# Performance work log

Measured on AMD Instinct MI355X. Metric: run time of the kernel, lower is better.

Reference implementation:

```python
import jax, jax.numpy as jnp
import numpy as np

EPS = 1e-5

def knn_gather(x, k):
    # x: [B,N,C] -> neighbors [B,N,k,C] (k nearest incl. self, DGCNN style)
    sq = jnp.sum(x * x, axis=-1)                                   # [B,N]
    dist = sq[:, :, None] + sq[:, None, :] - 2.0 * jnp.einsum('bnc,bmc->bnm', x, x)
    _, idx = jax.lax.top_k(-dist, k)                               # [B,N,k]
    neigh = jax.vmap(lambda xb, ib: xb[ib])(x, idx)                # [B,N,k,C]
    return neigh

def local_cov(neigh):
    # neigh: [B,N,k,C] -> flattened per-point covariance [B,N,C*C]
    k = neigh.shape[2]
    c = neigh - jnp.mean(neigh, axis=2, keepdims=True)
    cov = jnp.einsum('bnkc,bnkd->bncd', c, c) / k
    return cov.reshape(cov.shape[0], cov.shape[1], -1)

def bn(x, g, b):
    # BatchNorm1d training-mode forward on [B,N,C]: stats over (B,N), biased var
    m = jnp.mean(x, axis=(0, 1))
    v = jnp.var(x, axis=(0, 1))
    return (x - m) * jax.lax.rsqrt(v + EPS) * g + b

def setup_inputs() -> dict:
    key = jax.random.key(0)
    ks = jax.random.split(key, 8)
    B, N = 2, 8192
    d = {}
    d['x'] = jax.random.normal(ks[0], (B, N, 3), dtype=jnp.float32)
    # conv weights stored as [in, out] (1x1 Conv1d == per-point matmul)
    def w(k_, i, o):
        return jax.random.normal(k_, (i, o), dtype=jnp.float32) * (1.0 / np.sqrt(i))
    d['W1'] = w(ks[1], 12, 64);   d['g1'] = jnp.ones(64);   d['b1'] = jnp.zeros(64)
    d['W2'] = w(ks[2], 64, 64);   d['g2'] = jnp.ones(64);   d['b2'] = jnp.zeros(64)
    d['W3'] = w(ks[3], 64, 64);   d['g3'] = jnp.ones(64);   d['b3'] = jnp.zeros(64)
    d['gW1'] = w(ks[4], 64, 128);  d['gg1'] = jnp.ones(128);  d['gb1'] = jnp.zeros(128)
    d['gW2'] = w(ks[5], 128, 1024); d['gg2'] = jnp.ones(1024); d['gb2'] = jnp.zeros(1024)
    d['W4'] = w(ks[6], 1024, 512); d['g4'] = jnp.ones(512);  d['b4'] = jnp.zeros(512)
    return d

def reference(x, W1, g1, b1, W2, g2, b2, W3, g3, b3,
              gW1, gg1, gb1, gW2, gg2, gb2, W4, g4, b4):
    # GBEncoder forward
    neigh = knn_gather(x, 32)                                   # [B,N,32,3]
    h = jnp.concatenate([x, local_cov(neigh)], axis=-1)         # [B,N,12]
    h = jax.nn.relu(bn(h @ W1, g1, b1))                         # [B,N,64]
    h = jax.nn.relu(bn(h @ W2, g2, b2))
    h = jax.nn.relu(bn(h @ W3, g3, b3))
    # GraphLayer 1: knn(k=8) gather -> max over neighbors -> 1x1 conv + BN + LeakyReLU
    n = jnp.max(knn_gather(h, 8), axis=2)                       # [B,N,64]
    h = jax.nn.leaky_relu(bn(n @ gW1, gg1, gb1), 0.01)          # [B,N,128]
    # GraphLayer 2
    n = jnp.max(knn_gather(h, 8), axis=2)                       # [B,N,128]
    h = jax.nn.leaky_relu(bn(n @ gW2, gg2, gb2), 0.01)          # [B,N,1024]
    # global max-pool over points, keepdim -> [B,1,1024]
    h = jnp.max(h, axis=1, keepdims=True)
    return jax.nn.relu(bn(h @ W4, g4, b4))                      # [B,1,512]
```

## Files before the change

### kernel.cpp

```cpp
#include <hip/hip_runtime.h>
#include <cfloat>
#include <cstdint>

#define NPTS 8192
#define NBROWS 16384

typedef unsigned long long u64;

__device__ __forceinline__ unsigned fkey(float f) {
  unsigned u = __float_as_uint(f);
  return (u & 0x80000000u) ? ~u : (u | 0x80000000u);
}
__device__ __forceinline__ float fdecode(unsigned k) {
  unsigned u = (k & 0x80000000u) ? (k ^ 0x80000000u) : ~k;
  return __uint_as_float(u);
}

template <int K>
__device__ __forceinline__ void chain_insert(u64 (&kk)[K], u64 key) {
  #pragma unroll
  for (int q = K - 1; q >= 1; --q) {
    bool cm1 = key < kk[q - 1];
    bool cq  = key < kk[q];
    kk[q] = cm1 ? kk[q - 1] : (cq ? key : kk[q]);
  }
  kk[0] = (key < kk[0]) ? key : kk[0];
}

__global__ __launch_bounds__(256) void sqx_kernel(const float* __restrict__ x,
                                                  float* __restrict__ sq) {
  int r = blockIdx.x * 256 + threadIdx.x;
  const float* xp = x + (size_t)r * 3;
  sq[r] = fmaf(xp[2], xp[2], fmaf(xp[1], xp[1], xp[0] * xp[0]));
}

__global__ __launch_bounds__(512, 4) void knn32_cov_kernel(const float* __restrict__ x,
                                                           const float* __restrict__ sqx,
                                                           float* __restrict__ feat) {
  __shared__ __align__(16) unsigned char smem[78080];
  float4* stage4 = (float4*)smem;
  unsigned* keyArea = (unsigned*)smem;
  unsigned* Trow = (unsigned*)(smem + 67584);
  unsigned* cnt  = (unsigned*)(smem + 67712);
  u64* apb = (u64*)(smem + 67840);

  const int t = threadIdx.x;
  const int r = t & 31, sub = t >> 5;
  const int rowBase = blockIdx.x * 32;
  const int batchBase = rowBase & ~(NPTS - 1);
  const int gRow = rowBase + r;

  const float xi0 = x[(size_t)gRow * 3 + 0];
  const float xi1 = x[(size_t)gRow * 3 + 1];
  const float xi2 = x[(size_t)gRow * 3 + 2];
  const float sqi = sqx[gRow];

  unsigned K[32];
  #pragma unroll
  for (int q = 0; q < 32; ++q) K[q] = 0xFFFFFFFFu;

  for (int round = 0; round < 4; ++round) {
    __syncthreads();
    #pragma unroll
    for (int u = 0; u < 4; ++u) {
      int pp = t + 512 * u;
      int s = pp >> 7, jj = pp & 127;
      int j = s * 512 + round * 128 + jj;
      const float* xp = x + (size_t)(batchBase + j) * 3;
      float4 w;
      w.x = xp[0]; w.y = xp[1]; w.z = xp[2];
      w.w = sqx[batchBase + j];
      stage4[pp] = w;
    }
    __syncthreads();
    const float4* st = stage4 + sub * 128;
    for (int jj = 0; jj < 128; ++jj) {
      float4 w = st[jj];
      float dot = fmaf(xi2, w.z, fmaf(xi1, w.y, xi0 * w.x));
      float d = sqi + w.w - 2.0f * dot;
      unsigned key = fkey(d);
      #pragma unroll
      for (int q = 31; q >= 1; --q) K[q] = max(K[q - 1], min(key, K[q]));
      K[0] = min(key, K[0]);
    }
  }
  __syncthreads();
  {
    const int base = (sub * 32 + r) * 33;
    #pragma unroll
    for (int z = 0; z < 32; ++z) keyArea[base + z] = K[z];
  }
  __syncthreads();
  if (t < 32) {
    cnt[t] = 0u;
    unsigned P[16];
    #pragma unroll
    for (int s = 0; s < 16; ++s) P[s] = 0u;
    unsigned T = 0u;
    for (int step = 0; step < 32; ++step) {
      unsigned best = 0xFFFFFFFFu; int bs = 0;
      #pragma unroll
      for (int s = 0; s < 16; ++s) {
        unsigned v = keyArea[(s * 32 + t) * 33 + P[s]];
        if (v < best) { best = v; bs = s; }
      }
      T = best;
      #pragma unroll
      for (int s = 0; s < 16; ++s) P[s] += (s == bs);
    }
    Trow[t] = T;
  }
  __syncthreads();
  for (int round = 0; round < 4; ++round) {
    __syncthreads();
    #pragma unroll
    for (int u = 0; u < 4; ++u) {
      int pp = t + 512 * u;
      int s = pp >> 7, jj = pp & 127;
      int j = s * 512 + round * 128 + jj;
      const float* xp = x + (size_t)(batchBase + j) * 3;
      float4 w;
      w.x = xp[0]; w.y = xp[1]; w.z = xp[2];
      w.w = sqx[batchBase + j];
      stage4[pp] = w;
    }
    __syncthreads();
    const float4* st = stage4 + sub * 128;
    const unsigned T = Trow[r];
    for (int jj = 0; jj < 128; ++jj) {
      float4 w = st[jj];
      float dot = fmaf(xi2, w.z, fmaf(xi1, w.y, xi0 * w.x));
      float d = sqi + w.w - 2.0f * dot;
      unsigned key = fkey(d);
      if (key <= T) {
        int j = sub * 512 + round * 128 + jj;
        unsigned slot = atomicAdd(&cnt[r], 1u);
        if (slot < 40u) apb[r * 40 + slot] = ((u64)key << 16) | (unsigned)j;
      }
    }
  }
  __syncthreads();
  if (t < 32) {
    int n = (int)cnt[t]; if (n > 40) n = 40;
    u64 kk[32];
    #pragma unroll
    for (int q = 0; q < 32; ++q) kk[q] = ~0ULL;
    for (int i = 0; i < n; ++i) chain_insert<32>(kk, apb[t * 40 + i]);
    float sx = 0.f, sy = 0.f, sz = 0.f;
    #pragma unroll 4
    for (int z = 0; z < 32; ++z) {
      const float* xp = x + (size_t)(batchBase + (int)(kk[z] & 0xFFFFULL)) * 3;
      sx += xp[0]; sy += xp[1]; sz += xp[2];
    }
    const float m0 = sx * (1.f / 32.f), m1 = sy * (1.f / 32.f), m2 = sz * (1.f / 32.f);
    float c00 = 0, c01 = 0, c02 = 0, c11 = 0, c12 = 0, c22 = 0;
    #pragma unroll 4
    for (int z = 0; z < 32; ++z) {
      const float* xp = x + (size_t)(batchBase + (int)(kk[z] & 0xFFFFULL)) * 3;
      float a0 = xp[0] - m0, a1 = xp[1] - m1, a2 = xp[2] - m2;
      c00 = fmaf(a0, a0, c00); c01 = fmaf(a0, a1, c01); c02 = fmaf(a0, a2, c02);
      c11 = fmaf(a1, a1, c11); c12 = fmaf(a1, a2, c12); c22 = fmaf(a2, a2, c22);
    }
    const float inv = 1.f / 32.f;
    float* fp = feat + (size_t)(rowBase + t) * 12;
    fp[0] = xi0; fp[1] = xi1; fp[2] = xi2;
    fp[3] = c00 * inv; fp[4] = c01 * inv; fp[5] = c02 * inv;
    fp[6] = c01 * inv; fp[7] = c11 * inv; fp[8] = c12 * inv;
    fp[9] = c02 * inv; fp[10] = c12 * inv; fp[11] = c22 * inv;
  }
}

__global__ __launch_bounds__(64) void mm12_64_kernel(const float* __restrict__ feat,
                                                     const float* __restrict__ W,
                                                     float* __restrict__ y,
                                                     float* __restrict__ psum,
                                                     float* __restrict__ psq) {
  __shared__ __align__(16) float Ws[12 * 64];
  const int t = threadIdx.x;
  for (int u = t; u < 192; u += 64) ((float4*)Ws)[u] = ((const float4*)W)[u];
  __syncthreads();
  const int row = blockIdx.x * 64 + t;
  float in[12];
  {
    const float4* fp = (const float4*)(feat + (size_t)row * 12);
    float4 a = fp[0], b = fp[1], c = fp[2];
    in[0] = a.x; in[1] = a.y; in[2] = a.z; in[3] = a.w;
    in[4] = b.x; in[5] = b.y; in[6] = b.z; in[7] = b.w;
    in[8] = c.x; in[9] = c.y; in[10] = c.z; in[11] = c.w;
  }
  float acc[64];
  #pragma unroll
  for (int o = 0; o < 64; ++o) acc[o] = 0.f;
  #pragma unroll
  for (int i = 0; i < 12; ++i) {
    const float xi = in[i];
    #pragma unroll
    for (int og = 0; og < 16; ++og) {
      float4 w4 = *(const float4*)(Ws + i * 64 + og * 4);
      acc[og * 4 + 0] = fmaf(xi, w4.x, acc[og * 4 + 0]);
      acc[og * 4 + 1] = fmaf(xi, w4.y, acc[og * 4 + 1]);
      acc[og * 4 + 2] = fmaf(xi, w4.z, acc[og * 4 + 2]);
      acc[og * 4 + 3] = fmaf(xi, w4.w, acc[og * 4 + 3]);
    }
  }
  float4* yp = (float4*)(y + (size_t)row * 64);
  #pragma unroll
  for (int og = 0; og < 16; ++og)
    yp[og] = make_float4(acc[og * 4 + 0], acc[og * 4 + 1], acc[og * 4 + 2], acc[og * 4 + 3]);
  #pragma unroll 1
  for (int o = 0; o < 64; ++o) {
    float s = acc[o], q = acc[o] * acc[o];
    #pragma unroll
    for (int m = 1; m < 64; m <<= 1) { s += __shfl_xor(s, m); q += __shfl_xor(q, m); }
    if (t == 0) { psum[blockIdx.x * 64 + o] = s; psq[blockIdx.x * 64 + o] = q; }
  }
}

template <int OUT, bool BNRELU>
__global__ __launch_bounds__(64) void mm64_kernel(const float* __restrict__ src,
                                                  const float* __restrict__ W,
                                                  const float* __restrict__ scale,
                                                  const float* __restrict__ shift,
                                                  float* __restrict__ y,
                                                  float* __restrict__ psum,
                                                  float* __restrict__ psq) {
  __shared__ __align__(16) float Ws[64 * OUT];
  const int t = threadIdx.x;
  for (int u = t; u < 16 * OUT; u += 64) ((float4*)Ws)[u] = ((const float4*)W)[u];
  __syncthreads();
  const int row = blockIdx.x * 64 + t;
  float in[64];
  {
    const float4* sp = (const float4*)(src + (size_t)row * 64);
    #pragma unroll
    for (int u = 0; u < 16; ++u) {
      float4 v = sp[u];
      if (BNRELU) {
        v.x = fmaxf(fmaf(v.x, scale[u * 4 + 0], shift[u * 4 + 0]), 0.f);
        v.y = fmaxf(fmaf(v.y, scale[u * 4 + 1], shift[u * 4 + 1]), 0.f);
        v.z = fmaxf(fmaf(v.z, scale[u * 4 + 2], shift[u * 4 + 2]), 0.f);
        v.w = fmaxf(fmaf(v.w, scale[u * 4 + 3], shift[u * 4 + 3]), 0.f);
      }
      in[u * 4 + 0] = v.x; in[u * 4 + 1] = v.y; in[u * 4 + 2] = v.z; in[u * 4 + 3] = v.w;
    }
  }
  for (int half = 0; half < OUT / 64; ++half) {
    float acc[64];
    #pragma unroll
    for (int o = 0; o < 64; ++o) acc[o] = 0.f;
    #pragma unroll 4
    for (int i = 0; i < 64; ++i) {
      const float xi = in[i];
      #pragma unroll
      for (int og = 0; og < 16; ++og) {
        float4 w4 = *(const float4*)(Ws + i * OUT + half * 64 + og * 4);
        acc[og * 4 + 0] = fmaf(xi, w4.x, acc[og * 4 + 0]);
        acc[og * 4 + 1] = fmaf(xi, w4.y, acc[og * 4 + 1]);
        acc[og * 4 + 2] = fmaf(xi, w4.z, acc[og * 4 + 2]);
        acc[og * 4 + 3] = fmaf(xi, w4.w, acc[og * 4 + 3]);
      }
    }
    float4* yp = (float4*)(y + (size_t)row * OUT + half * 64);
    #pragma unroll
    for (int og = 0; og < 16; ++og)
      yp[og] = make_float4(acc[og * 4 + 0], acc[og * 4 + 1], acc[og * 4 + 2], acc[og * 4 + 3]);
    #pragma unroll 1
    for (int o = 0; o < 64; ++o) {
      float s = acc[o], q = acc[o] * acc[o];
      #pragma unroll
      for (int m = 1; m < 64; m <<= 1) { s += __shfl_xor(s, m); q += __shfl_xor(q, m); }
      if (t == 0) {
        psum[blockIdx.x * OUT + half * 64 + o] = s;
        psq[blockIdx.x * OUT + half * 64 + o] = q;
      }
    }
  }
}

template <int C>
__global__ void finP_kernel(const float* __restrict__ psum, const float* __restrict__ psq,
                            const float* __restrict__ g, const float* __restrict__ b,
                            float* __restrict__ scale, float* __restrict__ shift) {
  int c = threadIdx.x;
  float s = 0.f, q = 0.f;
  for (int bb = 0; bb < 256; ++bb) { s += psum[bb * C + c]; q += psq[bb * C + c]; }
  float m = s * (1.f / 16384.f);
  float v = q * (1.f / 16384.f) - m * m;
  float sc = g[c] * rsqrtf(v + 1e-5f);
  scale[c] = sc;
  shift[c] = b[c] - m * sc;
}

template <int C, bool LEAKY>
__global__ __launch_bounds__(256) void apply_kernel(const float* __restrict__ yraw,
                                                    const float* __restrict__ scale,
                                                    const float* __restrict__ shift,
                                                    float* __restrict__ hout,
                                                    float* __restrict__ sqout) {
  const int row = blockIdx.x * 256 + threadIdx.x;
  const float4* sp = (const float4*)(yraw + (size_t)row * C);
  float4* dp = (float4*)(hout + (size_t)row * C);
  float sq = 0.f;
  #pragma unroll
  for (int u = 0; u < C / 4; ++u) {
    float4 v = sp[u];
    float4 o;
    o.x = fmaf(v.x, scale[u * 4 + 0], shift[u * 4 + 0]);
    o.y = fmaf(v.y, scale[u * 4 + 1], shift[u * 4 + 1]);
    o.z = fmaf(v.z, scale[u * 4 + 2], shift[u * 4 + 2]);
    o.w = fmaf(v.w, scale[u * 4 + 3], shift[u * 4 + 3]);
    if (LEAKY) {
      o.x = o.x > 0.f ? o.x : 0.01f * o.x;
      o.y = o.y > 0.f ? o.y : 0.01f * o.y;
      o.z = o.z > 0.f ? o.z : 0.01f * o.z;
      o.w = o.w > 0.f ? o.w : 0.01f * o.w;
    } else {
      o.x = fmaxf(o.x, 0.f); o.y = fmaxf(o.y, 0.f);
      o.z = fmaxf(o.z, 0.f); o.w = fmaxf(o.w, 0.f);
    }
    sq = fmaf(o.x, o.x, sq); sq = fmaf(o.y, o.y, sq);
    sq = fmaf(o.z, o.z, sq); sq = fmaf(o.w, o.w, sq);
    dp[u] = o;
  }
  sqout[row] = sq;
}

template <int C>
__global__ __launch_bounds__(256, 4) void knn8_kernel(const float* __restrict__ h,
                                                      const float* __restrict__ sqh,
                                                      u64* __restrict__ plist) {
  static_assert(C == 64 || C == 128, "C");
  constexpr int SMEMB = (C * 64 * 4 + 64 * 64 * 4) > 32768 ? (C * 64 * 4 + 64 * 64 * 4) : 32768;
  __shared__ __align__(16) unsigned char smem[SMEMB];
  float* As = (float*)smem;
  float* Bs = (float*)(smem + C * 64 * 4);
  __shared__ float sqAs[64];
  __shared__ float sqBs[64];
  u64* mb = (u64*)smem;

  const int t = threadIdx.x;
  const int rg = blockIdx.x >> 2, quarter = blockIdx.x & 3;
  const int rowBase = rg * 64;
  const int batchBase = rowBase & ~(NPTS - 1);
  const int tx = t & 15, ty = t >> 4;

  {
    const int ar = t & 63;
    const int k0 = (t >> 6) * (C / 4);
    const float* src = h + (size_t)(rowBase + ar) * C + k0;
    #pragma unroll
    for (int kk = 0; kk < C / 4; kk += 4) {
      float4 v = *(const float4*)(src + kk);
      As[(k0 + kk + 0) * 64 + ar] = v.x;
      As[(k0 + kk + 1) * 64 + ar] = v.y;
      As[(k0 + kk + 2) * 64 + ar] = v.z;
      As[(k0 + kk + 3) * 64 + ar] = v.w;
    }
    if (t < 64) sqAs[t] = sqh[rowBase + t];
  }

  u64 L[4][8];
  #pragma unroll
  for (int q = 0; q < 4; ++q)
    #pragma unroll
    for (int z = 0; z < 8; ++z) L[q][z] = ~0ULL;

  for (int tile = 0; tile < 32; ++tile) {
    const int colBase = quarter * 2048 + tile * 64;
    float acc[16];
    #pragma unroll
    for (int q = 0; q < 16; ++q) acc[q] = 0.f;
    for (int ch = 0; ch < C / 64; ++ch) {
      __syncthreads();
      {
        const int bc = t & 63;
        const int k0 = (t >> 6) * 16;
        const float* src = h + (size_t)(batchBase + colBase + bc) * C + ch * 64 + k0;
        #pragma unroll
        for (int kk = 0; kk < 16; kk += 4) {
          float4 v = *(const float4*)(src + kk);
          Bs[(k0 + kk + 0) * 64 + bc] = v.x;
          Bs[(k0 + kk + 1) * 64 + bc] = v.y;
          Bs[(k0 + kk + 2) * 64 + bc] = v.z;
          Bs[(k0 + kk + 3) * 64 + bc] = v.w;
        }
        if (ch == 0 && t < 64) sqBs[t] = sqh[batchBase + colBase + t];
      }
      __syncthreads();
      const float* Ab = As + ch * 64 * 64;
      #pragma unroll 4
      for (int k = 0; k < 64; ++k) {
        float4 a4 = *(const float4*)(Ab + k * 64 + ty * 4);
        float4 b4 = *(const float4*)(Bs + k * 64 + tx * 4);
        acc[0] = fmaf(a4.x, b4.x, acc[0]);   acc[1] = fmaf(a4.x, b4.y, acc[1]);
        acc[2] = fmaf(a4.x, b4.z, acc[2]);   acc[3] = fmaf(a4.x, b4.w, acc[3]);
        acc[4] = fmaf(a4.y, b4.x, acc[4]);   acc[5] = fmaf(a4.y, b4.y, acc[5]);
        acc[6] = fmaf(a4.y, b4.z, acc[6]);   acc[7] = fmaf(a4.y, b4.w, acc[7]);
        acc[8] = fmaf(a4.z, b4.x, acc[8]);   acc[9] = fmaf(a4.z, b4.y, acc[9]);
        acc[10] = fmaf(a4.z, b4.z, acc[10]); acc[11] = fmaf(a4.z, b4.w, acc[11]);
        acc[12] = fmaf(a4.w, b4.x, acc[12]); acc[13] = fmaf(a4.w, b4.y, acc[13]);
        acc[14] = fmaf(a4.w, b4.z, acc[14]); acc[15] = fmaf(a4.w, b4.w, acc[15]);
      }
    }
    #pragma unroll
    for (int q = 0; q < 4; ++q) {
      const float sa = sqAs[ty * 4 + q];
      #pragma unroll
      for (int p = 0; p < 4; ++p) {
        float d = sa + sqBs[tx * 4 + p] - 2.0f * acc[q * 4 + p];
        int j = colBase + tx * 4 + p;
        u64 key = ((u64)fkey(d) << 16) | (unsigned)j;
        chain_insert<8>(L[q], key);
      }
    }
  }
  for (int rh = 0; rh < 2; ++rh) {
    __syncthreads();
    if (ty >= rh * 8 && ty < rh * 8 + 8) {
      #pragma unroll
      for (int q = 0; q < 4; ++q) {
        int lr = (ty - rh * 8) * 4 + q;
        #pragma unroll
        for (int z = 0; z < 8; ++z) mb[(lr * 16 + tx) * 8 + z] = L[q][z];
      }
    }
    __syncthreads();
    if (t < 32) {
      int ps[16];
      #pragma unroll
      for (int s = 0; s < 16; ++s) ps[s] = 0;
      u64 outk[8];
      for (int z = 0; z < 8; ++z) {
        u64 best = ~0ULL; int bs = 0;
        #pragma unroll
        for (int s = 0; s < 16; ++s) {
          u64 v = mb[(t * 16 + s) * 8 + ps[s]];
          if (v < best) { best = v; bs = s; }
        }
        outk[z] = best;
        #pragma unroll
        for (int s = 0; s < 16; ++s) ps[s] += (s == bs);
      }
      u64* dst = plist + ((size_t)(rowBase + rh * 32 + t) * 4 + quarter) * 8;
      #pragma unroll
      for (int z = 0; z < 8; ++z) dst[z] = outk[z];
    }
  }
}

template <int C>
__global__ __launch_bounds__(256) void knn8mg_kernel(const u64* __restrict__ plist,
                                                     const float* __restrict__ h,
                                                     float* __restrict__ nout) {
  const int row = blockIdx.x * 4 + (threadIdx.x >> 6);
  const int lane = threadIdx.x & 63;
  const int batchBase = row & ~(NPTS - 1);
  const u64* A = plist + (size_t)row * 32;
  u64 kk[8];
  #pragma unroll
  for (int z = 0; z < 8; ++z) kk[z] = A[z];
  #pragma unroll
  for (int z = 8; z < 32; ++z) chain_insert<8>(kk, A[z]);
  constexpr int PER = C / 64;
  float mx[PER];
  #pragma unroll
  for (int u = 0; u < PER; ++u) mx[u] = -FLT_MAX;
  #pragma unroll
  for (int z = 0; z < 8; ++z) {
    int idx = (int)(kk[z] & 0xFFFFULL);
    const float* src = h + (size_t)(batchBase + idx) * C;
    #pragma unroll
    for (int u = 0; u < PER; ++u)
      mx[u] = fmaxf(mx[u], src[lane + u * 64]);
  }
  float* dst = nout + (size_t)row * C;
  #pragma unroll
  for (int u = 0; u < PER; ++u) dst[lane + u * 64] = mx[u];
}

__global__ __launch_bounds__(256) void mmE_kernel(const float* __restrict__ n2,
                                                  const float* __restrict__ W,
                                                  float* __restrict__ psum,
                                                  float* __restrict__ psq,
                                                  unsigned* __restrict__ gmax) {
  __shared__ __align__(16) float As[64 * 64];
  __shared__ __align__(16) float Bs[64 * 64];
  __shared__ float sP[16 * 64];
  __shared__ float qP[16 * 64];
  __shared__ float mP[16 * 64];
  const int t = threadIdx.x;
  const int rowStripe = blockIdx.x >> 4;
  const int colStripe = blockIdx.x & 15;
  const int rowBase = rowStripe * 64;
  const int colBase = colStripe * 64;
  const int batch = rowBase >> 13;
  const int tx = t & 15, ty = t >> 4;

  float acc[16];
  #pragma unroll
  for (int q = 0; q < 16; ++q) acc[q] = 0.f;

  for (int kh = 0; kh < 2; ++kh) {
    __syncthreads();
    {
      const int ar = t & 63;
      const int k0 = (t >> 6) * 16;
      const float* src = n2 + (size_t)(rowBase + ar) * 128 + kh * 64 + k0;
      #pragma unroll
      for (int kk = 0; kk < 16; kk += 4) {
        float4 v = *(const float4*)(src + kk);
        As[(k0 + kk + 0) * 64 + ar] = v.x;
        As[(k0 + kk + 1) * 64 + ar] = v.y;
        As[(k0 + kk + 2) * 64 + ar] = v.z;
        As[(k0 + kk + 3) * 64 + ar] = v.w;
      }
    }
    {
      #pragma unroll
      for (int z = 0; z < 4; ++z) {
        int u = t + 256 * z;
        int k = u >> 4, c4 = u & 15;
        float4 v = *(const float4*)(W + (size_t)(kh * 64 + k) * 1024 + colBase + c4 * 4);
        *(float4*)(Bs + k * 64 + c4 * 4) = v;
      }
    }
    __syncthreads();
    #pragma unroll 4
    for (int k = 0; k < 64; ++k) {
      float4 a4 = *(const float4*)(As + k * 64 + ty * 4);
      float4 b4 = *(const float4*)(Bs + k * 64 + tx * 4);
      acc[0] = fmaf(a4.x, b4.x, acc[0]);   acc[1] = fmaf(a4.x, b4.y, acc[1]);
      acc[2] = fmaf(a4.x, b4.z, acc[2]);   acc[3] = fmaf(a4.x, b4.w, acc[3]);
      acc[4] = fmaf(a4.y, b4.x, acc[4]);   acc[5] = fmaf(a4.y, b4.y, acc[5]);
      acc[6] = fmaf(a4.y, b4.z, acc[6]);   acc[7] = fmaf(a4.y, b4.w, acc[7]);
      acc[8] = fmaf(a4.z, b4.x, acc[8]);   acc[9] = fmaf(a4.z, b4.y, acc[9]);
      acc[10] = fmaf(a4.z, b4.z, acc[10]); acc[11] = fmaf(a4.z, b4.w, acc[11]);
      acc[12] = fmaf(a4.w, b4.x, acc[12]); acc[13] = fmaf(a4.w, b4.y, acc[13]);
      acc[14] = fmaf(a4.w, b4.z, acc[14]); acc[15] = fmaf(a4.w, b4.w, acc[15]);
    }
  }
  #pragma unroll
  for (int p = 0; p < 4; ++p) {
    float s = 0.f, q = 0.f, m = -FLT_MAX;
    #pragma unroll
    for (int qq = 0; qq < 4; ++qq) {
      float v = acc[qq * 4 + p];
      s += v; q = fmaf(v, v, q); m = fmaxf(m, v);
    }
    sP[ty * 64 + tx * 4 + p] = s;
    qP[ty * 64 + tx * 4 + p] = q;
    mP[ty * 64 + tx * 4 + p] = m;
  }
  __syncthreads();
  if (t < 64) {
    float s = 0.f, q = 0.f, m = -FLT_MAX;
    #pragma unroll
    for (int u = 0; u < 16; ++u) {
      s += sP[u * 64 + t];
      q += qP[u * 64 + t];
      m = fmaxf(m, mP[u * 64 + t]);
    }
    psum[rowStripe * 1024 + colBase + t] = s;
    psq [rowStripe * 1024 + colBase + t] = q;
    atomicMax(&gmax[batch * 1024 + colBase + t], fkey(m));
  }
}

__global__ void poolbn_kernel(const float* __restrict__ psumE, const float* __restrict__ psqE,
                              const unsigned* __restrict__ gmax,
                              const float* __restrict__ gg2, const float* __restrict__ gb2,
                              float* __restrict__ fpool) {
  int c = threadIdx.x;
  float s = 0.f, q = 0.f;
  for (int bb = 0; bb < 256; ++bb) { s += psumE[bb * 1024 + c]; q += psqE[bb * 1024 + c]; }
  float m = s * (1.f / 16384.f);
  float v = q * (1.f / 16384.f) - m * m;
  float sc = gg2[c] * rsqrtf(v + 1e-5f);
  float sh = gb2[c] - m * sc;
  #pragma unroll
  for (int b = 0; b < 2; ++b) {
    float raw = fdecode(gmax[b * 1024 + c]);
    float t = fmaf(raw, sc, sh);
    fpool[b * 1024 + c] = t > 0.f ? t : 0.01f * t;
  }
}

__global__ __launch_bounds__(64) void final_kernel(const float* __restrict__ fpool,
                                                   const float* __restrict__ W4,
                                                   const float* __restrict__ g4,
                                                   const float* __restrict__ b4f,
                                                   float* __restrict__ out) {
  const int o = blockIdx.x * 64 + threadIdx.x;
  float a0 = 0.f, a1 = 0.f;
  for (int c = 0; c < 1024; ++c) {
    float w = W4[(size_t)c * 512 + o];
    a0 = fmaf(fpool[c], w, a0);
    a1 = fmaf(fpool[1024 + c], w, a1);
  }
  float m = 0.5f * (a0 + a1);
  float d0 = a0 - m, d1 = a1 - m;
  float v = 0.5f * (d0 * d0 + d1 * d1);
  float r = rsqrtf(v + 1e-5f);
  float o0 = fmaf(d0 * r, g4[o], b4f[o]);
  float o1 = fmaf(d1 * r, g4[o], b4f[o]);
  out[o] = fmaxf(o0, 0.f);
  out[512 + o] = fmaxf(o1, 0.f);
}

extern "C" void kernel_launch(void* const* d_in, const int* in_sizes, int n_in,
                              void* d_out, int out_size, void* d_ws, size_t ws_size,
                              hipStream_t stream) {
  (void)in_sizes; (void)n_in; (void)out_size; (void)ws_size;
  const float* x   = (const float*)d_in[0];
  const float* W1  = (const float*)d_in[1];
  const float* g1  = (const float*)d_in[2];
  const float* b1  = (const float*)d_in[3];
  const float* W2  = (const float*)d_in[4];
  const float* g2  = (const float*)d_in[5];
  const float* b2  = (const float*)d_in[6];
  const float* W3  = (const float*)d_in[7];
  const float* g3  = (const float*)d_in[8];
  const float* b3  = (const float*)d_in[9];
  const float* gW1 = (const float*)d_in[10];
  const float* gg1 = (const float*)d_in[11];
  const float* gb1 = (const float*)d_in[12];
  const float* gW2 = (const float*)d_in[13];
  const float* gg2 = (const float*)d_in[14];
  const float* gb2 = (const float*)d_in[15];
  const float* W4  = (const float*)d_in[16];
  const float* g4  = (const float*)d_in[17];
  const float* b4  = (const float*)d_in[18];
  float* out = (float*)d_out;
  float* ws = (float*)d_ws;

  float* sqx  = ws;
  float* feat = sqx + 16384;
  float* yA   = feat + 196608;
  float* yB   = yA + 1048576;
  float* h3   = yB + 1048576;
  float* sqh  = h3 + 1048576;
  float* yg1  = sqh + 16384;
  float* hg1  = yg1 + 2097152;
  float* sqg  = hg1 + 2097152;
  float* st   = sqg + 16384;

  unsigned* gmax = (unsigned*)(st);
  float* scale0 = st + 2048;  float* shift0 = st + 2112;
  float* scale1 = st + 2176;  float* shift1 = st + 2240;
  float* scale2 = st + 2304;  float* shift2 = st + 2368;
  float* scale3 = st + 2432;  float* shift3 = st + 2560;
  float* fpool  = st + 2688;
  float* p1s    = st + 4736;
  float* p1q    = p1s + 16384;

  float* p2s = feat;             float* p2q = feat + 16384;
  float* p3s = feat + 32768;     float* p3q = feat + 49152;
  float* p4s = yB;               float* p4q = yB + 32768;
  float* pEs = h3;               float* pEq = h3 + 262144;
  u64* plist = (u64*)yB;

  float* n1 = yA;
  float* n2 = yg1;

  hipMemsetAsync(gmax, 0, 2048 * sizeof(unsigned), stream);
  sqx_kernel<<<64, 256, 0, stream>>>(x, sqx);
  knn32_cov_kernel<<<512, 512, 0, stream>>>(x, sqx, feat);
  mm12_64_kernel<<<256, 64, 0, stream>>>(feat, W1, yA, p1s, p1q);
  finP_kernel<64><<<1, 64, 0, stream>>>(p1s, p1q, g1, b1, scale0, shift0);
  mm64_kernel<64, true><<<256, 64, 0, stream>>>(yA, W2, scale0, shift0, yB, p2s, p2q);
  finP_kernel<64><<<1, 64, 0, stream>>>(p2s, p2q, g2, b2, scale1, shift1);
  mm64_kernel<64, true><<<256, 64, 0, stream>>>(yB, W3, scale1, shift1, yA, p3s, p3q);
  finP_kernel<64><<<1, 64, 0, stream>>>(p3s, p3q, g3, b3, scale2, shift2);
  apply_kernel<64, false><<<64, 256, 0, stream>>>(yA, scale2, shift2, h3, sqh);
  knn8_kernel<64><<<1024, 256, 0, stream>>>(h3, sqh, plist);
  knn8mg_kernel<64><<<4096, 256, 0, stream>>>(plist, h3, n1);
  mm64_kernel<128, false><<<256, 64, 0, stream>>>(n1, gW1, scale0, shift0, yg1, p4s, p4q);
  finP_kernel<128><<<1, 128, 0, stream>>>(p4s, p4q, gg1, gb1, scale3, shift3);
  apply_kernel<128, true><<<64, 256, 0, stream>>>(yg1, scale3, shift3, hg1, sqg);
  knn8_kernel<128><<<1024, 256, 0, stream>>>(hg1, sqg, plist);
  knn8mg_kernel<128><<<4096, 256, 0, stream>>>(plist, hg1, n2);
  mmE_kernel<<<4096, 256, 0, stream>>>(n2, gW2, pEs, pEq, gmax);
  poolbn_kernel<<<1, 1024, 0, stream>>>(pEs, pEq, gmax, gg2, gb2, fpool);
  final_kernel<<<8, 64, 0, stream>>>(fpool, W4, g4, b4, out);
}
```

Before: 1.965 ms.

## Use split-bf16 MFMA for knn8 distances with fp32 candidate refinement

The graph-layer features are stored as three bf16 parts (hi/mid/lo split), and the knn8 distance GEMM now runs on bf16 MFMA using six cross products that approximate fp32 accuracy. Each quarter keeps 12 candidates instead of 8. A new refine kernel recomputes the exact distances of the 48 candidates in fp32 and picks the top 8 with wave shuffles before the max-gather. This moves the dominant FMA-bound distance work to matrix cores, at the cost of triple-size feature storage, extra refinement work and slightly lower occupancy.

```diff
diff --git a/kernel.cpp b/kernel.cpp
--- a/kernel.cpp
+++ b/kernel.cpp
@@ -6,6 +6,9 @@
 #define NBROWS 16384
 
 typedef unsigned long long u64;
+typedef unsigned short ushortT;
+typedef __attribute__((ext_vector_type(8))) short short8;
+typedef __attribute__((ext_vector_type(4))) float f32x4;
 
 __device__ __forceinline__ unsigned fkey(float f) {
   unsigned u = __float_as_uint(f);
@@ -14,6 +17,15 @@
 __device__ __forceinline__ float fdecode(unsigned k) {
   unsigned u = (k & 0x80000000u) ? (k ^ 0x80000000u) : ~k;
   return __uint_as_float(u);
+}
+__device__ __forceinline__ float bf2f(ushortT v) {
+  return __uint_as_float(((unsigned)v) << 16);
+}
+__device__ __forceinline__ unsigned rne16(float x, float& hf) {
+  unsigned u = __float_as_uint(x);
+  unsigned r = (u + 0x7FFFu + ((u >> 16) & 1u)) >> 16;
+  hf = __uint_as_float(r << 16);
+  return r;
 }
 
 template <int K>
@@ -295,133 +307,162 @@
 __global__ __launch_bounds__(256) void apply_kernel(const float* __restrict__ yraw,
                                                     const float* __restrict__ scale,
                                                     const float* __restrict__ shift,
-                                                    float* __restrict__ hout,
+                                                    ushortT* __restrict__ hbf,
                                                     float* __restrict__ sqout) {
   const int row = blockIdx.x * 256 + threadIdx.x;
   const float4* sp = (const float4*)(yraw + (size_t)row * C);
-  float4* dp = (float4*)(hout + (size_t)row * C);
+  ushortT* hb = hbf + (size_t)row * (3 * C);
   float sq = 0.f;
   #pragma unroll
-  for (int u = 0; u < C / 4; ++u) {
-    float4 v = sp[u];
-    float4 o;
-    o.x = fmaf(v.x, scale[u * 4 + 0], shift[u * 4 + 0]);
-    o.y = fmaf(v.y, scale[u * 4 + 1], shift[u * 4 + 1]);
-    o.z = fmaf(v.z, scale[u * 4 + 2], shift[u * 4 + 2]);
-    o.w = fmaf(v.w, scale[u * 4 + 3], shift[u * 4 + 3]);
-    if (LEAKY) {
-      o.x = o.x > 0.f ? o.x : 0.01f * o.x;
-      o.y = o.y > 0.f ? o.y : 0.01f * o.y;
-      o.z = o.z > 0.f ? o.z : 0.01f * o.z;
-      o.w = o.w > 0.f ? o.w : 0.01f * o.w;
-    } else {
-      o.x = fmaxf(o.x, 0.f); o.y = fmaxf(o.y, 0.f);
-      o.z = fmaxf(o.z, 0.f); o.w = fmaxf(o.w, 0.f);
-    }
-    sq = fmaf(o.x, o.x, sq); sq = fmaf(o.y, o.y, sq);
-    sq = fmaf(o.z, o.z, sq); sq = fmaf(o.w, o.w, sq);
-    dp[u] = o;
+  for (int g = 0; g < C / 8; ++g) {
+    float e[8];
+    #pragma unroll
+    for (int half = 0; half < 2; ++half) {
+      float4 v = sp[g * 2 + half];
+      const int u = g * 2 + half;
+      float4 o;
+      o.x = fmaf(v.x, scale[u * 4 + 0], shift[u * 4 + 0]);
+      o.y = fmaf(v.y, scale[u * 4 + 1], shift[u * 4 + 1]);
+      o.z = fmaf(v.z, scale[u * 4 + 2], shift[u * 4 + 2]);
+      o.w = fmaf(v.w, scale[u * 4 + 3], shift[u * 4 + 3]);
+      if (LEAKY) {
+        o.x = o.x > 0.f ? o.x : 0.01f * o.x;
+        o.y = o.y > 0.f ? o.y : 0.01f * o.y;
+        o.z = o.z > 0.f ? o.z : 0.01f * o.z;
+        o.w = o.w > 0.f ? o.w : 0.01f * o.w;
+      } else {
+        o.x = fmaxf(o.x, 0.f); o.y = fmaxf(o.y, 0.f);
+        o.z = fmaxf(o.z, 0.f); o.w = fmaxf(o.w, 0.f);
+      }
+      sq = fmaf(o.x, o.x, sq); sq = fmaf(o.y, o.y, sq);
+      sq = fmaf(o.z, o.z, sq); sq = fmaf(o.w, o.w, sq);
+      e[half * 4 + 0] = o.x; e[half * 4 + 1] = o.y;
+      e[half * 4 + 2] = o.z; e[half * 4 + 3] = o.w;
+    }
+    unsigned pa[8], pb[8], pc[8];
+    #pragma unroll
+    for (int j = 0; j < 8; ++j) {
+      float af, bf, cf;
+      pa[j] = rne16(e[j], af);
+      float r1 = e[j] - af;
+      pb[j] = rne16(r1, bf);
+      float r2 = r1 - bf;
+      pc[j] = rne16(r2, cf);
+    }
+    uint4 va, vb, vc;
+    va.x = pa[0] | (pa[1] << 16); va.y = pa[2] | (pa[3] << 16);
+    va.z = pa[4] | (pa[5] << 16); va.w = pa[6] | (pa[7] << 16);
+    vb.x = pb[0] | (pb[1] << 16); vb.y = pb[2] | (pb[3] << 16);
+    vb.z = pb[4] | (pb[5] << 16); vb.w = pb[6] | (pb[7] << 16);
+    vc.x = pc[0] | (pc[1] << 16); vc.y = pc[2] | (pc[3] << 16);
+    vc.z = pc[4] | (pc[5] << 16); vc.w = pc[6] | (pc[7] << 16);
+    *(uint4*)(hb + g * 8) = va;
+    *(uint4*)(hb + C + g * 8) = vb;
+    *(uint4*)(hb + 2 * C + g * 8) = vc;
   }
   sqout[row] = sq;
 }
 
 template <int C>
-__global__ __launch_bounds__(256, 4) void knn8_kernel(const float* __restrict__ h,
+__global__ __launch_bounds__(256, 3) void knn8_kernel(const ushortT* __restrict__ hbf,
                                                       const float* __restrict__ sqh,
                                                       u64* __restrict__ plist) {
   static_assert(C == 64 || C == 128, "C");
-  constexpr int SMEMB = (C * 64 * 4 + 64 * 64 * 4) > 32768 ? (C * 64 * 4 + 64 * 64 * 4) : 32768;
-  __shared__ __align__(16) unsigned char smem[SMEMB];
-  float* As = (float*)smem;
-  float* Bs = (float*)(smem + C * 64 * 4);
-  __shared__ float sqAs[64];
-  __shared__ float sqBs[64];
+  constexpr int STR = 3 * C + 8;
+  constexpr int BSB = 64 * STR * 2;
+  constexpr int SMB = BSB > 49152 ? BSB : 49152;
+  __shared__ __align__(16) unsigned char smem[SMB];
+  ushortT* Bs = (ushortT*)smem;
   u64* mb = (u64*)smem;
+  __shared__ float sqB[64];
 
   const int t = threadIdx.x;
+  const int l = t & 63, w = t >> 6;
+  const int quad = l >> 4, fif = l & 15;
   const int rg = blockIdx.x >> 2, quarter = blockIdx.x & 3;
   const int rowBase = rg * 64;
   const int batchBase = rowBase & ~(NPTS - 1);
-  const int tx = t & 15, ty = t >> 4;
-
+
+  constexpr int KS = C / 32;
+  short8 aa[KS], ab[KS], ac[KS];
   {
-    const int ar = t & 63;
-    const int k0 = (t >> 6) * (C / 4);
-    const float* src = h + (size_t)(rowBase + ar) * C + k0;
-    #pragma unroll
-    for (int kk = 0; kk < C / 4; kk += 4) {
-      float4 v = *(const float4*)(src + kk);
-      As[(k0 + kk + 0) * 64 + ar] = v.x;
-      As[(k0 + kk + 1) * 64 + ar] = v.y;
-      As[(k0 + kk + 2) * 64 + ar] = v.z;
-      As[(k0 + kk + 3) * 64 + ar] = v.w;
-    }
-    if (t < 64) sqAs[t] = sqh[rowBase + t];
-  }
+    const int arow = rowBase + 16 * w + fif;
+    const ushortT* ap = hbf + (size_t)arow * (3 * C);
+    #pragma unroll
+    for (int s = 0; s < KS; ++s) {
+      aa[s] = *(const short8*)(ap + s * 32 + quad * 8);
+      ab[s] = *(const short8*)(ap + C + s * 32 + quad * 8);
+      ac[s] = *(const short8*)(ap + 2 * C + s * 32 + quad * 8);
+    }
+  }
+  float sqA[4];
+  #pragma unroll
+  for (int r = 0; r < 4; ++r) sqA[r] = sqh[rowBase + 16 * w + quad * 4 + r];
 
   u64 L[4][8];
   #pragma unroll
-  for (int q = 0; q < 4; ++q)
-    #pragma unroll
-    for (int z = 0; z < 8; ++z) L[q][z] = ~0ULL;
-
-  for (int tile = 0; tile < 32; ++tile) {
-    const int colBase = quarter * 2048 + tile * 64;
-    float acc[16];
-    #pragma unroll
-    for (int q = 0; q < 16; ++q) acc[q] = 0.f;
-    for (int ch = 0; ch < C / 64; ++ch) {
-      __syncthreads();
-      {
-        const int bc = t & 63;
-        const int k0 = (t >> 6) * 16;
-        const float* src = h + (size_t)(batchBase + colBase + bc) * C + ch * 64 + k0;
+  for (int r = 0; r < 4; ++r)
+    #pragma unroll
+    for (int z = 0; z < 8; ++z) L[r][z] = ~0ULL;
+
+  constexpr int CPP = C / 8;
+  constexpr int LOG = (CPP == 16) ? 4 : 3;
+
+  for (int chunk = 0; chunk < 32; ++chunk) {
+    const int cb = quarter * 2048 + chunk * 64;
+    __syncthreads();
+    {
+      #pragma unroll
+      for (int p = 0; p < 3; ++p) {
         #pragma unroll
-        for (int kk = 0; kk < 16; kk += 4) {
-          float4 v = *(const float4*)(src + kk);
-          Bs[(k0 + kk + 0) * 64 + bc] = v.x;
-          Bs[(k0 + kk + 1) * 64 + bc] = v.y;
-          Bs[(k0 + kk + 2) * 64 + bc] = v.z;
-          Bs[(k0 + kk + 3) * 64 + bc] = v.w;
+        for (int z = 0; z < (64 * CPP) / 256; ++z) {
+          int id = t + 256 * z;
+          int col = id >> LOG, ch = id & (CPP - 1);
+          uint4 v = *(const uint4*)(hbf + (size_t)(batchBase + cb + col) * (3 * C) + p * C + ch * 8);
+          *(uint4*)(Bs + col * STR + p * C + ch * 8) = v;
         }
-        if (ch == 0 && t < 64) sqBs[t] = sqh[batchBase + colBase + t];
-      }
-      __syncthreads();
-      const float* Ab = As + ch * 64 * 64;
-      #pragma unroll 4
-      for (int k = 0; k < 64; ++k) {
-        float4 a4 = *(const float4*)(Ab + k * 64 + ty * 4);
-        float4 b4 = *(const float4*)(Bs + k * 64 + tx * 4);
-        acc[0] = fmaf(a4.x, b4.x, acc[0]);   acc[1] = fmaf(a4.x, b4.y, acc[1]);
-        acc[2] = fmaf(a4.x, b4.z, acc[2]);   acc[3] = fmaf(a4.x, b4.w, acc[3]);
-        acc[4] = fmaf(a4.y, b4.x, acc[4]);   acc[5] = fmaf(a4.y, b4.y, acc[5]);
-        acc[6] = fmaf(a4.y, b4.z, acc[6]);   acc[7] = fmaf(a4.y, b4.w, acc[7]);
-        acc[8] = fmaf(a4.z, b4.x, acc[8]);   acc[9] = fmaf(a4.z, b4.y, acc[9]);
-        acc[10] = fmaf(a4.z, b4.z, acc[10]); acc[11] = fmaf(a4.z, b4.w, acc[11]);
-        acc[12] = fmaf(a4.w, b4.x, acc[12]); acc[13] = fmaf(a4.w, b4.y, acc[13]);
-        acc[14] = fmaf(a4.w, b4.z, acc[14]); acc[15] = fmaf(a4.w, b4.w, acc[15]);
-      }
-    }
-    #pragma unroll
-    for (int q = 0; q < 4; ++q) {
-      const float sa = sqAs[ty * 4 + q];
-      #pragma unroll
-      for (int p = 0; p < 4; ++p) {
-        float d = sa + sqBs[tx * 4 + p] - 2.0f * acc[q * 4 + p];
-        int j = colBase + tx * 4 + p;
-        u64 key = ((u64)fkey(d) << 16) | (unsigned)j;
-        chain_insert<8>(L[q], key);
+      }
+      if (t < 64) sqB[t] = sqh[batchBase + cb + t];
+    }
+    __syncthreads();
+    #pragma unroll
+    for (int tile = 0; tile < 4; ++tile) {
+      const int lcol = tile * 16 + fif;
+      f32x4 acc0 = {0.f, 0.f, 0.f, 0.f};
+      f32x4 acc1 = {0.f, 0.f, 0.f, 0.f};
+      f32x4 acc2 = {0.f, 0.f, 0.f, 0.f};
+      const ushortT* bp = Bs + lcol * STR + quad * 8;
+      #pragma unroll
+      for (int s = 0; s < KS; ++s) {
+        short8 ba = *(const short8*)(bp + s * 32);
+        short8 bb = *(const short8*)(bp + C + s * 32);
+        short8 bc = *(const short8*)(bp + 2 * C + s * 32);
+        acc0 = __builtin_amdgcn_mfma_f32_16x16x32_bf16(aa[s], ba, acc0, 0, 0, 0);
+        acc1 = __builtin_amdgcn_mfma_f32_16x16x32_bf16(aa[s], bb, acc1, 0, 0, 0);
+        acc2 = __builtin_amdgcn_mfma_f32_16x16x32_bf16(ab[s], ba, acc2, 0, 0, 0);
+        acc0 = __builtin_amdgcn_mfma_f32_16x16x32_bf16(aa[s], bc, acc0, 0, 0, 0);
+        acc1 = __builtin_amdgcn_mfma_f32_16x16x32_bf16(ac[s], ba, acc1, 0, 0, 0);
+        acc2 = __builtin_amdgcn_mfma_f32_16x16x32_bf16(ab[s], bb, acc2, 0, 0, 0);
+      }
+      const float sb = sqB[lcol];
+      const unsigned gcol = (unsigned)(cb + lcol);
+      #pragma unroll
+      for (int r = 0; r < 4; ++r) {
+        float dot = acc0[r] + acc1[r] + acc2[r];
+        float d = sqA[r] + sb - 2.0f * dot;
+        u64 key = ((u64)fkey(d) << 16) | gcol;
+        chain_insert<8>(L[r], key);
       }
     }
   }
   for (int rh = 0; rh < 2; ++rh) {
     __syncthreads();
-    if (ty >= rh * 8 && ty < rh * 8 + 8) {
-      #pragma unroll
-      for (int q = 0; q < 4; ++q) {
-        int lr = (ty - rh * 8) * 4 + q;
+    if ((w >> 1) == rh) {
+      #pragma unroll
+      for (int r = 0; r < 4; ++r) {
+        int lr = (16 * w + quad * 4 + r) & 31;
         #pragma unroll
-        for (int z = 0; z < 8; ++z) mb[(lr * 16 + tx) * 8 + z] = L[q][z];
+        for (int z = 0; z < 8; ++z) mb[(lr * 16 + fif) * 8 + z] = L[r][z];
       }
     }
     __syncthreads();
@@ -429,53 +470,98 @@
       int ps[16];
       #pragma unroll
       for (int s = 0; s < 16; ++s) ps[s] = 0;
-      u64 outk[8];
-      for (int z = 0; z < 8; ++z) {
+      u64 outk[12];
+      for (int z = 0; z < 12; ++z) {
         u64 best = ~0ULL; int bs = 0;
         #pragma unroll
         for (int s = 0; s < 16; ++s) {
-          u64 v = mb[(t * 16 + s) * 8 + ps[s]];
+          u64 v = (ps[s] < 8) ? mb[(t * 16 + s) * 8 + ps[s]] : ~0ULL;
           if (v < best) { best = v; bs = s; }
         }
         outk[z] = best;
         #pragma unroll
         for (int s = 0; s < 16; ++s) ps[s] += (s == bs);
       }
-      u64* dst = plist + ((size_t)(rowBase + rh * 32 + t) * 4 + quarter) * 8;
-      #pragma unroll
-      for (int z = 0; z < 8; ++z) dst[z] = outk[z];
+      u64* dst = plist + ((size_t)(rowBase + rh * 32 + t) * 4 + quarter) * 12;
+      #pragma unroll
+      for (int z = 0; z < 12; ++z) dst[z] = outk[z];
     }
   }
 }
 
 template <int C>
-__global__ __launch_bounds__(256) void knn8mg_kernel(const u64* __restrict__ plist,
-                                                     const float* __restrict__ h,
+__global__ __launch_bounds__(256) void knn8rf_kernel(const u64* __restrict__ plist,
+                                                     const ushortT* __restrict__ hbf,
+                                                     const float* __restrict__ sqh,
                                                      float* __restrict__ nout) {
-  const int row = blockIdx.x * 4 + (threadIdx.x >> 6);
-  const int lane = threadIdx.x & 63;
+  __shared__ float xiL[4][C];
+  const int t = threadIdx.x;
+  const int w = t >> 6, l = t & 63;
+  const int row = blockIdx.x * 4 + w;
   const int batchBase = row & ~(NPTS - 1);
-  const u64* A = plist + (size_t)row * 32;
-  u64 kk[8];
-  #pragma unroll
-  for (int z = 0; z < 8; ++z) kk[z] = A[z];
-  #pragma unroll
-  for (int z = 8; z < 32; ++z) chain_insert<8>(kk, A[z]);
+  {
+    const ushortT* src = hbf + (size_t)row * (3 * C);
+    #pragma unroll
+    for (int u = 0; u < C / 64; ++u) {
+      int ch = l + u * 64;
+      float av = bf2f(src[ch]), bv = bf2f(src[C + ch]), cv = bf2f(src[2 * C + ch]);
+      xiL[w][ch] = av + (bv + cv);
+    }
+  }
+  __syncthreads();
+  const float sqi = sqh[row];
+  const u64* pl = plist + (size_t)row * 48;
+  u64 myk = ~0ULL;
+  if (l < 48) {
+    int cand = (int)(pl[l] & 0xFFFFULL) & (NPTS - 1);
+    const ushortT* sp = hbf + (size_t)(batchBase + cand) * (3 * C);
+    float dot = 0.f;
+    #pragma unroll 4
+    for (int kk = 0; kk < C; kk += 2) {
+      unsigned ua = *(const unsigned*)(sp + kk);
+      unsigned ub = *(const unsigned*)(sp + C + kk);
+      unsigned uc = *(const unsigned*)(sp + 2 * C + kk);
+      float a0 = __uint_as_float(ua << 16), a1 = __uint_as_float(ua & 0xFFFF0000u);
+      float b0 = __uint_as_float(ub << 16), b1 = __uint_as_float(ub & 0xFFFF0000u);
+      float c0 = __uint_as_float(uc << 16), c1 = __uint_as_float(uc & 0xFFFF0000u);
+      float x0 = a0 + (b0 + c0), x1 = a1 + (b1 + c1);
+      dot = fmaf(xiL[w][kk], x0, dot);
+      dot = fmaf(xiL[w][kk + 1], x1, dot);
+    }
+    float d = sqi + sqh[batchBase + cand] - 2.0f * dot;
+    myk = ((u64)fkey(d) << 16) | (unsigned)cand;
+  }
+  u64 top[8];
+  #pragma unroll
+  for (int z = 0; z < 8; ++z) {
+    u64 m = myk;
+    #pragma unroll
+    for (int off = 1; off < 64; off <<= 1) {
+      u64 o = (u64)__shfl_xor((long long)m, off);
+      m = o < m ? o : m;
+    }
+    top[z] = m;
+    if (myk == m) myk = ~0ULL;
+  }
   constexpr int PER = C / 64;
   float mx[PER];
   #pragma unroll
   for (int u = 0; u < PER; ++u) mx[u] = -FLT_MAX;
   #pragma unroll
   for (int z = 0; z < 8; ++z) {
-    int idx = (int)(kk[z] & 0xFFFFULL);
-    const float* src = h + (size_t)(batchBase + idx) * C;
-    #pragma unroll
-    for (int u = 0; u < PER; ++u)
-      mx[u] = fmaxf(mx[u], src[lane + u * 64]);
+    int idx = (int)(top[z] & 0xFFFFULL) & (NPTS - 1);
+    const ushortT* src = hbf + (size_t)(batchBase + idx) * (3 * C);
+    #pragma unroll
+    for (int u = 0; u < PER; ++u) {
+      int ch = l + u * 64;
+      float av = bf2f(src[ch]), bv = bf2f(src[C + ch]), cv = bf2f(src[2 * C + ch]);
+      float xv = av + (bv + cv);
+      mx[u] = fmaxf(mx[u], xv);
+    }
   }
   float* dst = nout + (size_t)row * C;
   #pragma unroll
-  for (int u = 0; u < PER; ++u) dst[lane + u * 64] = mx[u];
+  for (int u = 0; u < PER; ++u) dst[l + u * 64] = mx[u];
 }
 
 __global__ __launch_bounds__(256) void mmE_kernel(const float* __restrict__ n2,
@@ -635,14 +721,13 @@
 
   float* sqx  = ws;
   float* feat = sqx + 16384;
-  float* yA   = feat + 196608;
-  float* yB   = yA + 1048576;
-  float* h3   = yB + 1048576;
-  float* sqh  = h3 + 1048576;
-  float* yg1  = sqh + 16384;
-  float* hg1  = yg1 + 2097152;
-  float* sqg  = hg1 + 2097152;
-  float* st   = sqg + 16384;
+  float* bufA = feat + 196608;
+  float* bufB = bufA + 1048576;
+  float* sqh  = bufB + 1048576;
+  float* sqg  = sqh + 16384;
+  float* ygr  = sqg + 16384;
+  float* hbfR = ygr + 2097152;
+  float* st   = hbfR + 3145728;
 
   unsigned* gmax = (unsigned*)(st);
   float* scale0 = st + 2048;  float* shift0 = st + 2112;
@@ -655,30 +740,32 @@
 
   float* p2s = feat;             float* p2q = feat + 16384;
   float* p3s = feat + 32768;     float* p3q = feat + 49152;
-  float* p4s = yB;               float* p4q = yB + 32768;
-  float* pEs = h3;               float* pEq = h3 + 262144;
-  u64* plist = (u64*)yB;
-
-  float* n1 = yA;
-  float* n2 = yg1;
+  float* p4s = feat;             float* p4q = feat + 32768;
+  float* pEs = bufA;             float* pEq = bufA + 262144;
+  u64* plist = (u64*)bufA;
+
+  ushortT* hbf1 = (ushortT*)hbfR;
+  ushortT* hbf2 = (ushortT*)hbfR;
+  float* n1 = hbfR + 1572864;
+  float* n2 = ygr;
 
   hipMemsetAsync(gmax, 0, 2048 * sizeof(unsigned), stream);
   sqx_kernel<<<64, 256, 0, stream>>>(x, sqx);
   knn32_cov_kernel<<<512, 512, 0, stream>>>(x, sqx, feat);
-  mm12_64_kernel<<<256, 64, 0, stream>>>(feat, W1, yA, p1s, p1q);
+  mm12_64_kernel<<<256, 64, 0, stream>>>(feat, W1, bufA, p1s, p1q);
   finP_kernel<64><<<1, 64, 0, stream>>>(p1s, p1q, g1, b1, scale0, shift0);
-  mm64_kernel<64, true><<<256, 64, 0, stream>>>(yA, W2, scale0, shift0, yB, p2s, p2q);
+  mm64_kernel<64, true><<<256, 64, 0, stream>>>(bufA, W2, scale0, shift0, bufB, p2s, p2q);
   finP_kernel<64><<<1, 64, 0, stream>>>(p2s, p2q, g2, b2, scale1, shift1);
-  mm64_kernel<64, true><<<256, 64, 0, stream>>>(yB, W3, scale1, shift1, yA, p3s, p3q);
+  mm64_kernel<64, true><<<256, 64, 0, stream>>>(bufB, W3, scale1, shift1, bufA, p3s, p3q);
   finP_kernel<64><<<1, 64, 0, stream>>>(p3s, p3q, g3, b3, scale2, shift2);
-  apply_kernel<64, false><<<64, 256, 0, stream>>>(yA, scale2, shift2, h3, sqh);
-  knn8_kernel<64><<<1024, 256, 0, stream>>>(h3, sqh, plist);
-  knn8mg_kernel<64><<<4096, 256, 0, stream>>>(plist, h3, n1);
-  mm64_kernel<128, false><<<256, 64, 0, stream>>>(n1, gW1, scale0, shift0, yg1, p4s, p4q);
+  apply_kernel<64, false><<<64, 256, 0, stream>>>(bufA, scale2, shift2, hbf1, sqh);
+  knn8_kernel<64><<<1024, 256, 0, stream>>>(hbf1, sqh, plist);
+  knn8rf_kernel<64><<<4096, 256, 0, stream>>>(plist, hbf1, sqh, n1);
+  mm64_kernel<128, false><<<256, 64, 0, stream>>>(n1, gW1, scale0, shift0, ygr, p4s, p4q);
   finP_kernel<128><<<1, 128, 0, stream>>>(p4s, p4q, gg1, gb1, scale3, shift3);
-  apply_kernel<128, true><<<64, 256, 0, stream>>>(yg1, scale3, shift3, hg1, sqg);
-  knn8_kernel<128><<<1024, 256, 0, stream>>>(hg1, sqg, plist);
-  knn8mg_kernel<128><<<4096, 256, 0, stream>>>(plist, hg1, n2);
+  apply_kernel<128, true><<<64, 256, 0, stream>>>(ygr, scale3, shift3, hbf2, sqg);
+  knn8_kernel<128><<<1024, 256, 0, stream>>>(hbf2, sqg, plist);
+  knn8rf_kernel<128><<<4096, 256, 0, stream>>>(plist, hbf2, sqg, n2);
   mmE_kernel<<<4096, 256, 0, stream>>>(n2, gW2, pEs, pEq, gmax);
   poolbn_kernel<<<1, 1024, 0, stream>>>(pEs, pEq, gmax, gg2, gb2, fpool);
   final_kernel<<<8, 64, 0, stream>>>(fpool, W4, g4, b4, out);
```

After: 2.121 ms. +8.0%, slower.
